# Optimization experiments

Hardware: AMD Instinct MI355X
Metric: run time of the kernel (lower is better)

The kernel has to match this reference:

```python
import jax, jax.numpy as jnp
import numpy as np

B, N, D = 16, 1024, 5
R_HID = 8  # radial MLP hidden width


def setup_inputs() -> dict:
    key = jax.random.key(0)
    ks = jax.random.split(key, 16)
    feats = jax.random.normal(ks[0], (B, N, D), jnp.float32)
    coors = 3.0 * jax.random.normal(ks[1], (B, N, 3), jnp.float32)
    a = jax.random.bernoulli(ks[2], 0.01, (B, N, N))
    adj_mat = a | jnp.swapaxes(a, 1, 2)
    s = 1.0 / np.sqrt(D)
    Wq = s * jax.random.normal(ks[3], (D, D), jnp.float32)
    Wk = s * jax.random.normal(ks[4], (D, D), jnp.float32)
    Wv = s * jax.random.normal(ks[5], (D, D), jnp.float32)
    Wo = s * jax.random.normal(ks[6], (D, D), jnp.float32)
    w_r1 = 0.5 * jax.random.normal(ks[7], (1, R_HID), jnp.float32)
    b_r1 = jnp.zeros((R_HID,), jnp.float32)
    w_r2 = 0.5 * jax.random.normal(ks[8], (R_HID, 1), jnp.float32)
    b_r2 = jnp.zeros((1,), jnp.float32)
    w1 = (1.0 / np.sqrt(D)) * jax.random.normal(ks[9], (D, 128), jnp.float32)
    b1 = jnp.zeros((128,), jnp.float32)
    w2 = (1.0 / np.sqrt(128.0)) * jax.random.normal(ks[10], (128, 3), jnp.float32)
    b2 = jnp.zeros((3,), jnp.float32)
    return dict(feats=feats, coors=coors, adj_mat=adj_mat, Wq=Wq, Wk=Wk, Wv=Wv,
                Wo=Wo, w_r1=w_r1, b_r1=b_r1, w_r2=w_r2, b_r2=b_r2,
                w1=w1, b1=b1, w2=w2, b2=b2)


def _se3_layer(feats, coors, neigh, Wq, Wk, Wv, Wo, w_r1, b_r1, w_r2, b_r2):
    # SE(3)-invariant sparse graph attention on degree-0 channels.
    # Attention logits = content term + radial (distance-only) bias, so the
    # scalar output is invariant to global rotations/translations of coors.
    q = jnp.einsum('bnd,de->bne', feats, Wq)
    k = jnp.einsum('bnd,de->bne', feats, Wk)
    v = jnp.einsum('bnd,de->bne', feats, Wv)
    rel = coors[:, :, None, :] - coors[:, None, :, :]        # [B,N,N,3]
    dist = jnp.sqrt(jnp.sum(rel * rel, axis=-1) + 1e-8)      # [B,N,N]
    h = jax.nn.relu(dist[..., None] * w_r1[0] + b_r1)        # [B,N,N,R_HID]
    rbias = (h @ w_r2)[..., 0] + b_r2[0]                     # [B,N,N]
    scores = jnp.einsum('bid,bjd->bij', q, k) / np.sqrt(q.shape[-1]) + rbias
    scores = jnp.where(neigh, scores, -1e9)
    attn = jax.nn.softmax(scores, axis=-1)
    agg = jnp.einsum('bij,bjd->bid', attn, v)
    return feats + jnp.einsum('bid,de->bie', agg, Wo)        # residual


def reference(feats, coors, adj_mat, Wq, Wk, Wv, Wo, w_r1, b_r1, w_r2, b_r2,
              w1, b1, w2, b2):
    a = adj_mat.astype(jnp.float32)
    # num_adj_degrees=2: attend over 1-hop and 2-hop neighbors (+ self)
    adj2 = jnp.einsum('bij,bjk->bik', a, a) > 0
    eye = jnp.eye(adj_mat.shape[1], dtype=bool)[None]
    neigh = adj_mat | adj2 | eye
    x = _se3_layer(feats, coors, neigh, Wq, Wk, Wv, Wo, w_r1, b_r1, w_r2, b_r2)
    pooled = jnp.mean(x, axis=1)                              # [B, D]
    hdn = jax.nn.relu(pooled @ w1 + b1)
    return hdn @ w2 + b2                                      # [B, 3]
```

## Files before the change

kernel.cpp:

```cpp
#include <hip/hip_runtime.h>
#include <hip/hip_bf16.h>

#define BB 16
#define NN 1024
#define DD 5
#define RH 8

typedef unsigned long long u64;
typedef unsigned int u32;
typedef __hip_bfloat16 bf16;

static __device__ __forceinline__ float tof(bf16 x) { return __bfloat162float(x); }
static __device__ __forceinline__ float ldf(const void* p, long long i, bool f) {
  return f ? ((const float*)p)[i] : tof(((const bf16*)p)[i]);
}

#define LOG2E 1.4426950408889634f
#define PACK_BLOCKS (BB * NN * 16 / 256)
#define KV_BLOCKS (BB * NN / 256)


__global__ __launch_bounds__(256) void k_pack(
    const void* __restrict__ adj, const void* __restrict__ feats,
    const void* __restrict__ coors,
    const void* __restrict__ Wk, const void* __restrict__ Wv,
    const void* __restrict__ Wo,
    u64* __restrict__ adjbits, float4* __restrict__ kvg,
    float* __restrict__ czg, int* __restrict__ gflags,
    float* __restrict__ pooled, int* __restrict__ cntr) {
  __shared__ int sNon01, sNonpair, sLow3;
  __shared__ int sCnt[4];
  __shared__ float wkL[25], wvL[25], woL[25];
  int tid = threadIdx.x;

  if (blockIdx.x >= PACK_BLOCKS) {
    int kb = blockIdx.x - PACK_BLOCKS;
    if (kb == 0) {
      if (tid < BB * DD) pooled[tid] = 0.0f;
      else if (tid < BB * DD + BB) cntr[tid - BB * DD] = 0;
    }
    {
      u32 x = ((const u32*)feats)[tid];
      u32 lo = x & 0xFFFFu;
      int e = (int)((lo >> 7) & 0xFFu);
      bool insane = !(lo == 0u || (e >= 90 && e <= 150));
      u64 m = __ballot(insane);
      if ((tid & 63) == 0) sCnt[tid >> 6] = (int)__popcll(m);
    }
    __syncthreads();
    bool f32 = (sCnt[0] + sCnt[1] + sCnt[2] + sCnt[3]) > 64;
    if (tid < 25) {
      wkL[tid] = ldf(Wk, tid, f32);
      wvL[tid] = ldf(Wv, tid, f32);
      woL[tid] = ldf(Wo, tid, f32);
    }
    if (kb == 0 && tid == 0) gflags[0] = f32 ? 1 : 0;
    __syncthreads();
    long long node = (long long)kb * 256 + tid;
    float f0 = ldf(feats, node * DD + 0, f32), f1 = ldf(feats, node * DD + 1, f32),
          f2 = ldf(feats, node * DD + 2, f32), f3 = ldf(feats, node * DD + 3, f32),
          f4 = ldf(feats, node * DD + 4, f32);
    float k[DD], tv[DD], v[DD];
    #pragma unroll
    for (int e = 0; e < DD; ++e) {
      k[e] = f0 * wkL[e] + f1 * wkL[5 + e] + f2 * wkL[10 + e] + f3 * wkL[15 + e] +
             f4 * wkL[20 + e];
      tv[e] = f0 * wvL[e] + f1 * wvL[5 + e] + f2 * wvL[10 + e] + f3 * wvL[15 + e] +
              f4 * wvL[20 + e];
    }
    #pragma unroll
    for (int e = 0; e < DD; ++e)
      v[e] = tv[0] * woL[e] + tv[1] * woL[5 + e] + tv[2] * woL[10 + e] +
             tv[3] * woL[15 + e] + tv[4] * woL[20 + e];
    float cx = ldf(coors, node * 3 + 0, f32);
    float cy = ldf(coors, node * 3 + 1, f32);
    float cz = ldf(coors, node * 3 + 2, f32);
    kvg[node * 3 + 0] = make_float4(k[0], k[1], k[2], k[3]);
    kvg[node * 3 + 1] = make_float4(k[4], v[0], v[1], v[2]);
    kvg[node * 3 + 2] = make_float4(v[3], v[4], cx, cy);
    czg[node] = cz;
    return;
  }

  if (tid == 0) { sNon01 = 0; sNonpair = 0; sLow3 = 0; }
  __syncthreads();
  {
    const u32* aw = (const u32*)adj;
    int non01 = 0, nonpair = 0, low3 = 0;
    for (int i = tid; i < 4096; i += 256) {
      u32 x = aw[i];
      u32 lo = x & 0xFFFFu, hi = x >> 16;
      non01 |= (x > 1u);
      nonpair |= !((lo == 0u || lo == 0x3F80u) && (hi == 0u || hi == 0x3F80u));
      low3 |= (lo == 0x3F80u);
    }
    if (non01) atomicOr(&sNon01, 1);
    if (nonpair) atomicOr(&sNonpair, 1);
    if (low3) atomicOr(&sLow3, 1);
  }
  __syncthreads();
  int mode;
  if (!sNon01) mode = 0;
  else if (!sNonpair) mode = sLow3 ? 2 : 3;
  else mode = 1;

  int gid = blockIdx.x * 256 + tid;
  int w = gid & 15;
  long long row = gid >> 4;
  long long base = row * NN + (long long)w * 64;
  u64 bits = 0;
  if (mode == 3) {
    const uint4* p = (const uint4*)((const float*)adj + base);
    #pragma unroll
    for (int t = 0; t < 16; ++t) {
      uint4 x = p[t];
      if (x.x << 1) bits |= 1ull << (4 * t + 0);
      if (x.y << 1) bits |= 1ull << (4 * t + 1);
      if (x.z << 1) bits |= 1ull << (4 * t + 2);
      if (x.w << 1) bits |= 1ull << (4 * t + 3);
    }
  } else if (mode == 0) {
    const uint4* p = (const uint4*)((const u32*)adj + base);
    #pragma unroll
    for (int t = 0; t < 16; ++t) {
      uint4 x = p[t];
      if (x.x) bits |= 1ull << (4 * t + 0);
      if (x.y) bits |= 1ull << (4 * t + 1);
      if (x.z) bits |= 1ull << (4 * t + 2);
      if (x.w) bits |= 1ull << (4 * t + 3);
    }
  } else if (mode == 2) {
    const uint4* p = (const uint4*)((const unsigned short*)adj + base);
    #pragma unroll
    for (int t = 0; t < 8; ++t) {
      uint4 x = p[t];
      u32 c[4] = {x.x, x.y, x.z, x.w};
      #pragma unroll
      for (int q = 0; q < 4; ++q) {
        if ((c[q] & 0x7FFFu)) bits |= 1ull << (8 * t + 2 * q + 0);
        if ((c[q] >> 16) & 0x7FFFu) bits |= 1ull << (8 * t + 2 * q + 1);
      }
    }
  } else {
    const uint4* p = (const uint4*)((const unsigned char*)adj + base);
    #pragma unroll
    for (int t = 0; t < 4; ++t) {
      uint4 x = p[t];
      u32 c[4] = {x.x, x.y, x.z, x.w};
      #pragma unroll
      for (int q = 0; q < 4; ++q)
        #pragma unroll
        for (int bb = 0; bb < 4; ++bb)
          if ((c[q] >> (8 * bb)) & 0xFFu) bits |= 1ull << (16 * t + 4 * q + bb);
    }
  }
  adjbits[gid] = bits;
}

__global__ __launch_bounds__(256) void k_attn(
    const void* __restrict__ feats, const void* __restrict__ coors,
    const void* __restrict__ Wq,
    const void* __restrict__ wr1, const void* __restrict__ br1,
    const void* __restrict__ wr2, const void* __restrict__ br2,
    const float4* __restrict__ kvg, const float* __restrict__ czg,
    const int* __restrict__ gflags, const u64* __restrict__ adjbits,
    float* __restrict__ pooled, int* __restrict__ cntr,
    const void* __restrict__ w1, const void* __restrict__ b1,
    const void* __restrict__ w2, const void* __restrict__ b2,
    float* __restrict__ out) {
  __shared__ unsigned short listL[4][NN];
  __shared__ u64 neighL[16][16];
  __shared__ float qL[16 * DD], ciL[16 * 3];
  __shared__ float wqL[25];
  __shared__ float wrL[3][RH];
  __shared__ float sConst[2];
  __shared__ int sFast, sLast;
  __shared__ float waveC[4][DD];
  __shared__ float pM[DD];
  __shared__ float hL[128];

  int bi = blockIdx.x;
  int b = bi >> 6, chunk = bi & 63;
  int tid = threadIdx.x;
  bool f32 = gflags[0] != 0;
  if (tid < 25) wqL[tid] = ldf(Wq, tid, f32);
  if (tid >= 64 && tid < 64 + RH) {
    int h = tid - 64;
    wrL[0][h] = ldf(wr1, h, f32);
    wrL[1][h] = ldf(br1, h, f32);
    wrL[2][h] = ldf(wr2, h, f32);
  }
  if (tid == 96) {
    float c = 0.0f;
    int ok = 1;
    #pragma unroll
    for (int h = 0; h < RH; ++h) {
      float w1h = ldf(wr1, h, f32);
      if (ldf(br1, h, f32) != 0.0f) ok = 0;
      if (w1h > 0.0f) c += w1h * ldf(wr2, h, f32);
    }
    sConst[0] = c * LOG2E;
    sConst[1] = ldf(br2, 0, f32) * LOG2E;
    sFast = ok;
  }
  __syncthreads();
  int fast = sFast;
  if (tid < 16) {
    long long row = (long long)b * NN + chunk * 16 + tid;
    float f0 = ldf(feats, row * DD + 0, f32), f1 = ldf(feats, row * DD + 1, f32),
          f2 = ldf(feats, row * DD + 2, f32), f3 = ldf(feats, row * DD + 3, f32),
          f4 = ldf(feats, row * DD + 4, f32);
    float qsc = fast ? (0.4472135954999579f * LOG2E) : 0.4472135954999579f;
    #pragma unroll
    for (int e = 0; e < DD; ++e)
      qL[tid * DD + e] = (f0 * wqL[e] + f1 * wqL[5 + e] + f2 * wqL[10 + e] +
                          f3 * wqL[15 + e] + f4 * wqL[20 + e]) * qsc;
    #pragma unroll
    for (int c = 0; c < 3; ++c)
      ciL[tid * 3 + c] = ldf(coors, row * 3 + c, f32);
  }
  __syncthreads();

  int g = tid >> 6, lane = tid & 63;
  int w = lane & 15, grp = lane >> 4;
  const u64* basep = adjbits + (size_t)b * NN * 16;
  for (int rr = 0; rr < 4; ++rr) {
    int il = g * 4 + rr;
    int i = chunk * 16 + il;
    u64 rw = basep[(size_t)i * 16 + w];
    unsigned short* list = listL[g];
    int cnt = 0;
    #pragma unroll
    for (int sw = 0; sw < 16; ++sw) {
      u64 bits = __shfl(rw, sw, 64);
      int mybit = (int)((bits >> lane) & 1ull);
      int pre = __popcll(bits & ((1ull << lane) - 1ull));
      if (mybit) list[cnt + pre] = (unsigned short)(sw * 64 + lane);
      cnt += __popcll(bits);
    }
    u64 acc = rw;
    if (w == (i >> 6)) acc |= 1ull << (i & 63);
    for (int n = grp; n < cnt; n += 4) acc |= basep[(size_t)list[n] * 16 + w];
    acc |= __shfl_xor(acc, 16, 64);
    acc |= __shfl_xor(acc, 32, 64);
    if (lane < 16) neighL[il][lane] = acc;
  }

  float q[4][DD], ci[4][3], l[4], A[4][DD];
  #pragma unroll
  for (int r = 0; r < 4; ++r) {
    #pragma unroll
    for (int e = 0; e < DD; ++e) q[r][e] = qL[(g * 4 + r) * DD + e];
    #pragma unroll
    for (int c = 0; c < 3; ++c) ci[r][c] = ciL[(g * 4 + r) * 3 + c];
    l[r] = 0.0f;
    #pragma unroll
    for (int e = 0; e < DD; ++e) A[r][e] = 0.0f;
  }
  const float4* kvb = kvg + (size_t)b * NN * 3;
  const float* czb = czg + (size_t)b * NN;
  float Cf = sConst[0], br2f = sConst[1];
  for (int it = 0; it < 16; ++it) {
    int j = it * 64 + lane;
    float4 ka = kvb[j * 3 + 0];
    float4 kb = kvb[j * 3 + 1];
    float4 kc = kvb[j * 3 + 2];
    float jx = kc.z, jy = kc.w, jz = czb[j];
    u64 nw[4];
    #pragma unroll
    for (int r = 0; r < 4; ++r) nw[r] = neighL[g * 4 + r][it];
    if (fast) {
      #pragma unroll
      for (int r = 0; r < 4; ++r) {
        float cx = jx - ci[r][0], cy = jy - ci[r][1], cz = jz - ci[r][2];
        float dist =
            __builtin_amdgcn_sqrtf(fmaf(cx, cx, fmaf(cy, cy, fmaf(cz, cz, 1e-8f))));
        float s = fmaf(q[r][0], ka.x, br2f);
        s = fmaf(q[r][1], ka.y, s);
        s = fmaf(q[r][2], ka.z, s);
        s = fmaf(q[r][3], ka.w, s);
        s = fmaf(q[r][4], kb.x, s);
        s = fmaf(Cf, dist, s);
        s = fminf(s, 126.0f);
        s = ((nw[r] >> lane) & 1ull) ? s : -150.0f;
        float p = __builtin_amdgcn_exp2f(s);
        l[r] += p;
        A[r][0] = fmaf(p, kb.y, A[r][0]);
        A[r][1] = fmaf(p, kb.z, A[r][1]);
        A[r][2] = fmaf(p, kb.w, A[r][2]);
        A[r][3] = fmaf(p, kc.x, A[r][3]);
        A[r][4] = fmaf(p, kc.y, A[r][4]);
      }
    } else {
      #pragma unroll
      for (int r = 0; r < 4; ++r) {
        float cx = jx - ci[r][0], cy = jy - ci[r][1], cz = jz - ci[r][2];
        float dist = sqrtf(fmaf(cx, cx, fmaf(cy, cy, fmaf(cz, cz, 1e-8f))));
        float rb = ldf(br2, 0, f32);
        #pragma unroll
        for (int h = 0; h < RH; ++h)
          rb += fmaxf(dist * wrL[0][h] + wrL[1][h], 0.0f) * wrL[2][h];
        float s = fmaf(q[r][0], ka.x, rb);
        s = fmaf(q[r][1], ka.y, s);
        s = fmaf(q[r][2], ka.z, s);
        s = fmaf(q[r][3], ka.w, s);
        s = fmaf(q[r][4], kb.x, s);
        s = fminf(s, 85.0f);
        s = ((nw[r] >> lane) & 1ull) ? s : -100.0f;
        float p = __expf(s);
        l[r] += p;
        A[r][0] = fmaf(p, kb.y, A[r][0]);
        A[r][1] = fmaf(p, kb.z, A[r][1]);
        A[r][2] = fmaf(p, kb.w, A[r][2]);
        A[r][3] = fmaf(p, kc.x, A[r][3]);
        A[r][4] = fmaf(p, kc.y, A[r][4]);
      }
    }
  }
  #pragma unroll
  for (int msk = 1; msk < 64; msk <<= 1) {
    #pragma unroll
    for (int r = 0; r < 4; ++r) {
      l[r] += __shfl_xor(l[r], msk, 64);
      A[r][0] += __shfl_xor(A[r][0], msk, 64);
      A[r][1] += __shfl_xor(A[r][1], msk, 64);
      A[r][2] += __shfl_xor(A[r][2], msk, 64);
      A[r][3] += __shfl_xor(A[r][3], msk, 64);
      A[r][4] += __shfl_xor(A[r][4], msk, 64);
    }
  }

  if (lane == 0) {
    float cw[DD] = {0.f, 0.f, 0.f, 0.f, 0.f};
    #pragma unroll
    for (int r = 0; r < 4; ++r) {
      long long grow = (long long)b * NN + chunk * 16 + g * 4 + r;
      float inv = (l[r] > 0.0f) ? 1.0f / l[r] : 0.0f;
      #pragma unroll
      for (int e = 0; e < DD; ++e)
        cw[e] += ldf(feats, grow * DD + e, f32) + A[r][e] * inv;
    }
    #pragma unroll
    for (int e = 0; e < DD; ++e) waveC[g][e] = cw[e];
  }
  __syncthreads();
  if (tid < DD) {
    float s = waveC[0][tid] + waveC[1][tid] + waveC[2][tid] + waveC[3][tid];
    float old = atomicAdd(&pooled[b * DD + tid], s);
    asm volatile("" :: "v"(old));
  }
  __syncthreads();
  if (tid == 0) sLast = (atomicAdd(&cntr[b], 1) == 63) ? 1 : 0;
  __syncthreads();

  if (sLast) {
    if (tid < DD) {
      float pv = __hip_atomic_load(&pooled[b * DD + tid], __ATOMIC_RELAXED,
                                   __HIP_MEMORY_SCOPE_AGENT);
      pM[tid] = pv * (1.0f / 1024.0f);
    }
    __syncthreads();
    if (tid < 128) {
      float acc = ldf(b1, tid, f32);
      #pragma unroll
      for (int d = 0; d < DD; ++d)
        acc = fmaf(pM[d], ldf(w1, d * 128 + tid, f32), acc);
      hL[tid] = fmaxf(acc, 0.0f);
    }
    __syncthreads();
    if (tid < 3) {
      float s = ldf(b2, tid, f32);
      for (int j = 0; j < 128; ++j)
        s = fmaf(hL[j], ldf(w2, j * 3 + tid, f32), s);
      out[b * 3 + tid] = s;
    }
  }
}

extern "C" void kernel_launch(void* const* d_in, const int* in_sizes, int n_in,
                              void* d_out, int out_size, void* d_ws, size_t ws_size,
                              hipStream_t stream) {
  const void* adj = d_in[2];
  float* out = (float*)d_out;

  char* w = (char*)d_ws;
  int* gflags = (int*)w;
  float* pooled = (float*)(w + 64);
  int* cntr = (int*)(w + 512);
  const size_t MB2 = (size_t)BB * NN * 16 * sizeof(u64);
  u64* adjbits = (u64*)(w + 1024);
  float4* kvg = (float4*)(w + 1024 + MB2);
  float* czg = (float*)(w + 1024 + MB2 + 786432);

  k_pack<<<PACK_BLOCKS + KV_BLOCKS, 256, 0, stream>>>(
      adj, d_in[0], d_in[1], d_in[4], d_in[5], d_in[6], adjbits, kvg, czg,
      gflags, pooled, cntr);
  k_attn<<<BB * 64, 256, 0, stream>>>(
      d_in[0], d_in[1], d_in[3], d_in[7], d_in[8], d_in[9], d_in[10], kvg, czg,
      gflags, adjbits, pooled, cntr, d_in[11], d_in[12], d_in[13], d_in[14],
      out);
}
```

Measured before the change: 191.8 us.

## Stage key/value tiles cooperatively in double-buffered LDS with register prefetch

Previously all four waves of a block each loaded the same 64-entry key/value/coordinate slice from global memory on every iteration. Now the block loads each 64-column tile once, spread across threads into registers, and writes it transposed into a double-buffered shared-memory tile. The next tile is prefetched while the current one is consumed. The redundant loads go away, at the cost of one block-wide barrier per iteration and extra LDS traffic. A now-unneeded early barrier is folded into the staging barrier.

```diff
diff --git a/kernel.cpp b/kernel.cpp
--- a/kernel.cpp
+++ b/kernel.cpp
@@ -168,6 +168,8 @@
     const void* __restrict__ w1, const void* __restrict__ b1,
     const void* __restrict__ w2, const void* __restrict__ b2,
     float* __restrict__ out) {
+  __shared__ __align__(16) float4 kvT[2][3][64];
+  __shared__ float czT[2][64];
   __shared__ unsigned short listL[4][NN];
   __shared__ u64 neighL[16][16];
   __shared__ float qL[16 * DD], ciL[16 * 3];
@@ -182,6 +184,14 @@
   int bi = blockIdx.x;
   int b = bi >> 6, chunk = bi & 63;
   int tid = threadIdx.x;
+
+  const float4* kvb3 = kvg + (size_t)b * NN * 3;
+  const float* czb = czg + (size_t)b * NN;
+  float4 stg;
+  float stgc;
+  if (tid < 192) stg = kvb3[tid];
+  else stgc = czb[tid - 192];
+
   bool f32 = gflags[0] != 0;
   if (tid < 25) wqL[tid] = ldf(Wq, tid, f32);
   if (tid >= 64 && tid < 64 + RH) {
@@ -219,7 +229,6 @@
     for (int c = 0; c < 3; ++c)
       ciL[tid * 3 + c] = ldf(coors, row * 3 + c, f32);
   }
-  __syncthreads();
 
   int g = tid >> 6, lane = tid & 63;
   int w = lane & 15, grp = lane >> 4;
@@ -246,6 +255,10 @@
     if (lane < 16) neighL[il][lane] = acc;
   }
 
+  if (tid < 192) kvT[0][tid % 3][tid / 3] = stg;
+  else czT[0][tid - 192] = stgc;
+  __syncthreads();
+
   float q[4][DD], ci[4][3], l[4], A[4][DD];
   #pragma unroll
   for (int r = 0; r < 4; ++r) {
@@ -257,18 +270,21 @@
     #pragma unroll
     for (int e = 0; e < DD; ++e) A[r][e] = 0.0f;
   }
-  const float4* kvb = kvg + (size_t)b * NN * 3;
-  const float* czb = czg + (size_t)b * NN;
   float Cf = sConst[0], br2f = sConst[1];
-  for (int it = 0; it < 16; ++it) {
-    int j = it * 64 + lane;
-    float4 ka = kvb[j * 3 + 0];
-    float4 kb = kvb[j * 3 + 1];
-    float4 kc = kvb[j * 3 + 2];
-    float jx = kc.z, jy = kc.w, jz = czb[j];
+  int cur = 0;
+  for (int t = 0; t < 16; ++t) {
+    if (t < 15) {
+      if (tid < 192) stg = kvb3[(size_t)(t + 1) * 192 + tid];
+      else stgc = czb[(t + 1) * 64 + (tid - 192)];
+    }
+    float4 ka = kvT[cur][0][lane];
+    float4 kb = kvT[cur][1][lane];
+    float4 kc = kvT[cur][2][lane];
+    float jz = czT[cur][lane];
+    float jx = kc.z, jy = kc.w;
     u64 nw[4];
     #pragma unroll
-    for (int r = 0; r < 4; ++r) nw[r] = neighL[g * 4 + r][it];
+    for (int r = 0; r < 4; ++r) nw[r] = neighL[g * 4 + r][t];
     if (fast) {
       #pragma unroll
       for (int r = 0; r < 4; ++r) {
@@ -316,6 +332,12 @@
         A[r][4] = fmaf(p, kc.y, A[r][4]);
       }
     }
+    if (t < 15) {
+      if (tid < 192) kvT[cur ^ 1][tid % 3][tid / 3] = stg;
+      else czT[cur ^ 1][tid - 192] = stgc;
+    }
+    __syncthreads();
+    cur ^= 1;
   }
   #pragma unroll
   for (int msk = 1; msk < 64; msk <<= 1) {
@@ -370,8 +392,8 @@
     __syncthreads();
     if (tid < 3) {
       float s = ldf(b2, tid, f32);
-      for (int j = 0; j < 128; ++j)
-        s = fmaf(hL[j], ldf(w2, j * 3 + tid, f32), s);
+      for (int j2 = 0; j2 < 128; ++j2)
+        s = fmaf(hL[j2], ldf(w2, j2 * 3 + tid, f32), s);
       out[b * 3 + tid] = s;
     }
   }
```

Result: no change. 190.2 us (-0.8%).
